# Optimization experiments

Measured on AMD Instinct MI355X. Metric: run time of the kernel, lower is better.

Reference implementation:

```python
import jax, jax.numpy as jnp
import numpy as np
from math import comb

# Implicit Bernstein form (BERN-NN-Implicit): a polynomial in V vars is a stack of
# term blocks; each term = V rows of univariate Bernstein coefficients, poly value
# = sum over terms of the product over vars of the univariate Bernstein polys.
N_IN, T_IN, V, DEG = 16, 64, 4, 4
C = DEG + 1          # coeffs per row at degree DEG
K = 2 * DEG + 1      # coeffs per row at degree 2*DEG (after squaring)

def _prod_matrix(d):
    # Bernstein product: (deg d) x (deg d) -> deg 2d ; c_k = sum_{i+j=k} b_i b_j C(d,i)C(d,j)/C(2d,k)
    M = np.zeros((d + 1, d + 1, 2 * d + 1), np.float32)
    for i in range(d + 1):
        for j in range(d + 1):
            M[i, j, i + j] = comb(d, i) * comb(d, j) / comb(2 * d, i + j)
    return jnp.asarray(M)

def _elev_matrix(d):
    # degree elevation d -> 2d : b'_j = sum_i b_i C(d,i)C(d,j-i)/C(2d,j)
    E = np.zeros((d + 1, 2 * d + 1), np.float32)
    for i in range(d + 1):
        for j in range(i, i + d + 1):
            E[i, j] = comb(d, i) * comb(d, j - i) / comb(2 * d, j)
    return jnp.asarray(E)

M_PROD = _prod_matrix(DEG)
E_ELEV = _elev_matrix(DEG)

def _scaled_terms(polys, w, idx):
    # mult_with_constant fused over all contributing inputs: scale row 0 of each term
    # block by the (nonzero) weight; concat of term blocks == sum_2_polys at equal degree.
    if idx.size == 0:
        return jnp.zeros((1, V, C), polys.dtype)  # zero polynomial (one zero term)
    sel = polys[idx]                                   # (n, T, V, C)
    sel = sel.at[:, :, 0, :].multiply(w[idx][:, None, None])
    return sel.reshape(-1, V, C)

def _add_const(P, c):
    # add_with_constant: append a constant term (Bernstein coeffs of a constant are all c)
    cols = P.shape[-1]
    row0 = c * jnp.ones((1, 1, cols), P.dtype)
    rest = jnp.ones((1, V - 1, cols), P.dtype)
    return jnp.concatenate([P, jnp.concatenate([row0, rest], axis=1)], axis=0)

def _ibf_minmax(P):
    # per-term interval = product over vars of [min,max] of each row; sum over terms
    lo = P.min(axis=-1); hi = P.max(axis=-1)           # (T, V)
    tlo, thi = lo[:, 0], hi[:, 0]
    for v in range(1, V):
        cands = jnp.stack([tlo * lo[:, v], tlo * hi[:, v], thi * lo[:, v], thi * hi[:, v]])
        tlo, thi = cands.min(0), cands.max(0)
    return tlo.sum(), thi.sum()

def _quad_of_poly(P, a, b, c):
    # a*p^2 + b*p + c in implicit Bernstein form; p^2 = all pairwise term products
    T = P.shape[0]
    sq = jnp.einsum('avi,bvj,ijk->abvk', P, P, M_PROD).reshape(T * T, V, K)
    sq = sq.at[:, 0, :].multiply(a)
    lin = jnp.einsum('tvi,ij->tvj', P, E_ELEV)          # elevate DEG -> 2*DEG
    lin = lin.at[:, 0, :].multiply(b)
    const = jnp.concatenate([c * jnp.ones((1, 1, K)), jnp.ones((1, V - 1, K))], axis=1)
    return jnp.concatenate([sq, lin, const], axis=0)

def _node_io(under_in, over_in, pos_w, neg_w, bias, pos_idx, neg_idx):
    under = jnp.concatenate([_scaled_terms(over_in, neg_w, neg_idx),
                             _scaled_terms(under_in, pos_w, pos_idx)], axis=0)
    under = _add_const(under, bias)
    over = jnp.concatenate([_scaled_terms(over_in, pos_w, pos_idx),
                            _scaled_terms(under_in, neg_w, neg_idx)], axis=0)
    over = _add_const(over, bias)
    return under, over

def setup_inputs() -> dict:
    key = jax.random.key(0)
    k1, k2, k3 = jax.random.split(key, 3)
    ui = 0.5 * jax.random.normal(k1, (N_IN, T_IN, V, C), jnp.float32)
    oi = ui + 0.05 * jnp.abs(jax.random.normal(k2, (N_IN, T_IN, V, C), jnp.float32))
    w = jax.random.normal(k3, (N_IN,), jnp.float32)
    return {
        'layer_inputs_under': ui,
        'layer_inputs_over': oi,
        'node_pos_weights': jnp.maximum(w, 0.0),
        'node_neg_weights': jnp.minimum(w, 0.0),
        'node_bias': jnp.asarray(-0.1, jnp.float32),
        'layer_inputs_under_degrees': jnp.full((N_IN, V), DEG, jnp.int32),
        'layer_inputs_over_degrees': jnp.full((N_IN, V), DEG, jnp.int32),
    }

def reference(layer_inputs_under, layer_inputs_over, node_pos_weights, node_neg_weights,
              node_bias, layer_inputs_under_degrees, layer_inputs_over_degrees):
    pos_idx = np.nonzero(np.asarray(node_pos_weights))[0]
    neg_idx = np.nonzero(np.asarray(node_neg_weights))[0]
    under, over = _node_io(layer_inputs_under, layer_inputs_over,
                           node_pos_weights, node_neg_weights, node_bias, pos_idx, neg_idx)
    deg = jnp.maximum(layer_inputs_under_degrees.astype(jnp.float32).max(0),
                      layer_inputs_over_degrees.astype(jnp.float32).max(0))  # (V,)
    l = _ibf_minmax(under)[0]
    u = _ibf_minmax(over)[1]
    lf, uf = float(l), float(u)   # host sync, mirrors the original's data-dependent branch
    if uf <= 0.0:
        return (jnp.zeros((1,)), jnp.zeros((1,)), jnp.zeros(V), jnp.zeros(V))
    if lf >= 0.0:
        return (under.reshape(-1, C), over.reshape(-1, C), deg, deg)
    # mixed case: sound quadratic relaxation of ReLU on [l, u]
    a, b, c = 1.0 / (-4.0 * l), 0.5, -l / 4.0   # upper: (x - l)^2 / (-4 l) >= relu(x)
    over_q = _quad_of_poly(over, a, b, c).reshape(-1, K)
    if uf >= -lf:
        # under relaxation = identity (coeffs [0,1,0])
        return (under.reshape(-1, C), over_q, deg, 2.0 * deg)
    # under relaxation = 0 (coeffs all zero)
    return (jnp.zeros((V, 1)), over_q, jnp.zeros(V), 2.0 * deg)
```

## Files before the change

### kernel.cpp

```cpp
#include <hip/hip_runtime.h>

#define NINP 16
#define TIN 64
#define NV 4
#define NC 5
#define NK 9
#define T_ROWS 1025
#define NPAIR (1025 * 1025)
#define UNDER_SZ (T_ROWS * NV * NC)
#define OQ_OFF UNDER_SZ
#define OQ_SQ_SZ (NPAIR * NV * NK)
#define TAIL_ELEMS ((T_ROWS + 1) * NV * NK)
#define DEG_OFF (OQ_OFF + OQ_SQ_SZ + TAIL_ELEMS)
#define WS_POVER 0
#define L_PART_LL 10252
#define FIXED_SCALE 16777216.0f

#define PREP_ELEM_BLOCKS 161
#define PREP_L_BLOCKS 4
#define PAIR_BLOCKS 4105
#define TAIL_BLOCKS 145

__device__ __forceinline__ int count_nz16(const float* __restrict__ w) {
    int c = 0;
#pragma unroll
    for (int n = 0; n < NINP; n++) c += (w[n] != 0.0f) ? 1 : 0;
    return c;
}

__device__ __forceinline__ int kth_nz16(const float* __restrict__ w, int k) {
    int c = 0, r = 0;
#pragma unroll
    for (int n = 0; n < NINP; n++) {
        bool nz = (w[n] != 0.0f);
        if (nz && c == k) r = n;
        c += nz ? 1 : 0;
    }
    return r;
}

__device__ __forceinline__ float under_val(const float* __restrict__ ui,
                                           const float* __restrict__ oi,
                                           const float* __restrict__ posw,
                                           const float* __restrict__ negw,
                                           float bias, int r, int v, int c) {
    if (r < 1024) {
        int g = r >> 6, tt = r & 63;
        int nNeg = count_nz16(negw);
        if (g < nNeg) {
            int n = kth_nz16(negw, g);
            return oi[((n * TIN + tt) * NV + v) * NC + c] * ((v == 0) ? negw[n] : 1.0f);
        }
        int n = kth_nz16(posw, g - nNeg);
        return ui[((n * TIN + tt) * NV + v) * NC + c] * ((v == 0) ? posw[n] : 1.0f);
    }
    return (v == 0) ? bias : 1.0f;
}

__global__ __launch_bounds__(256) void prep_kernel(
    const float* __restrict__ ui, const float* __restrict__ oi,
    const float* __restrict__ posw, const float* __restrict__ negw,
    const float* __restrict__ bias,
    const int* __restrict__ udeg, const int* __restrict__ odeg,
    float* __restrict__ out, float* __restrict__ ws) {
    const int bid = blockIdx.x;
    const int t = threadIdx.x;

    if (bid < PREP_ELEM_BLOCKS) {
        int gid = bid * 256 + t;
        if (gid < NV) {
            int m = 0;
            for (int n = 0; n < NINP; n++) {
                int a = udeg[n * NV + gid];
                int b = odeg[n * NV + gid];
                m = max(m, max(a, b));
            }
            out[DEG_OFF + gid] = (float)m;
            out[DEG_OFF + NV + gid] = 2.0f * (float)m;
        }
        if (gid < UNDER_SZ) {
            int r = gid / 20, rem = gid - r * 20, v = rem / 5, c = rem - v * 5;
            out[gid] = under_val(ui, oi, posw, negw, bias[0], r, v, c);
        } else if (gid < 2 * UNDER_SZ) {
            int e = gid - UNDER_SZ;
            int r = e / 20, rem = e - r * 20, v = rem / 5, c = rem - v * 5;
            float val;
            if (r < 1024) {
                int g = r >> 6, tt = r & 63;
                int nPos = count_nz16(posw);
                if (g < nPos) {
                    int n = kth_nz16(posw, g);
                    val = oi[((n * TIN + tt) * NV + v) * NC + c] * ((v == 0) ? posw[n] : 1.0f);
                } else {
                    int n = kth_nz16(negw, g - nPos);
                    val = ui[((n * TIN + tt) * NV + v) * NC + c] * ((v == 0) ? negw[n] : 1.0f);
                }
            } else {
                val = (v == 0) ? bias[0] : 1.0f;
            }
            ws[WS_POVER + e] = val;
        }
    } else {
        __shared__ long long s[256];
        const float b0 = bias[0];
        int r = (bid - PREP_ELEM_BLOCKS) * 256 + t;
        float tlo = 0.f, thi = 0.f;
#pragma unroll
        for (int v = 0; v < NV; v++) {
            float lo = under_val(ui, oi, posw, negw, b0, r, v, 0), hi = lo;
#pragma unroll
            for (int c = 1; c < NC; c++) {
                float x = under_val(ui, oi, posw, negw, b0, r, v, c);
                lo = fminf(lo, x);
                hi = fmaxf(hi, x);
            }
            if (v == 0) { tlo = lo; thi = hi; }
            else {
                float p0 = tlo * lo, p1 = tlo * hi, p2 = thi * lo, p3 = thi * hi;
                tlo = fminf(fminf(p0, p1), fminf(p2, p3));
                thi = fmaxf(fmaxf(p0, p1), fmaxf(p2, p3));
            }
        }
        long long acc = __float2ll_rn(tlo * FIXED_SCALE);
        if (bid == PREP_ELEM_BLOCKS && t == 0) {
            acc += __float2ll_rn(b0 * FIXED_SCALE);
        }
        s[t] = acc;
        __syncthreads();
        for (int off = 128; off > 0; off >>= 1) {
            if (t < off) s[t] += s[t + off];
            __syncthreads();
        }
        if (t == 0) ((long long*)ws)[L_PART_LL + (bid - PREP_ELEM_BLOCKS)] = s[0];
    }
}

__device__ __forceinline__ float c4_of(int j) {
    if (j == 0 || j == 4) return 1.f;
    if (j == 1 || j == 3) return 4.f;
    if (j == 2) return 6.f;
    return 0.f;
}

__global__ __launch_bounds__(256) void main_kernel(const float* __restrict__ P,
                                                   const long long* __restrict__ lpart,
                                                   float* __restrict__ out) {
    const int bid = blockIdx.x;
    const int t = threadIdx.x;
    const long long ll = lpart[0] + lpart[1] + lpart[2] + lpart[3];
    const float l = (float)ll * (1.0f / FIXED_SCALE);

    if (bid < PAIR_BLOCKS) {
        __shared__ float lds[256 * 37];
        const int p0 = bid * 256;
        int nvalid = NPAIR - p0;
        if (nvalid > 256) nvalid = 256;
        const float ascale = -0.25f / l;

        if (t < nvalid) {
            int p = p0 + t;
            int ai = p / 1025;
            int bi = p - ai * 1025;
            float pa[20], pb[20];
            const float4* A4 = reinterpret_cast<const float4*>(P + ai * 20);
            const float4* B4 = reinterpret_cast<const float4*>(P + bi * 20);
#pragma unroll
            for (int q = 0; q < 5; q++) {
                float4 x = A4[q];
                pa[4 * q] = x.x; pa[4 * q + 1] = x.y; pa[4 * q + 2] = x.z; pa[4 * q + 3] = x.w;
                float4 y = B4[q];
                pb[4 * q] = y.x; pb[4 * q + 1] = y.y; pb[4 * q + 2] = y.z; pb[4 * q + 3] = y.w;
            }
            const float C4[5] = {1.f, 4.f, 6.f, 4.f, 1.f};
            const float invC8[9] = {1.f, 0.125f, 1.f / 28.f, 1.f / 56.f, 1.f / 70.f,
                                    1.f / 56.f, 1.f / 28.f, 0.125f, 1.f};
#pragma unroll
            for (int v = 0; v < NV; v++) {
                float a_[5], b_[5];
#pragma unroll
                for (int i = 0; i < 5; i++) {
                    a_[i] = pa[v * 5 + i] * C4[i];
                    b_[i] = pb[v * 5 + i] * C4[i];
                }
                float cc[9];
#pragma unroll
                for (int k = 0; k < 9; k++) cc[k] = 0.f;
#pragma unroll
                for (int i = 0; i < 5; i++)
#pragma unroll
                    for (int j = 0; j < 5; j++) cc[i + j] += a_[i] * b_[j];
                const float sc = (v == 0) ? ascale : 1.0f;
#pragma unroll
                for (int k = 0; k < 9; k++) lds[t * 37 + v * 9 + k] = cc[k] * invC8[k] * sc;
            }
        }
        __syncthreads();

        const int nf4 = nvalid * 9;
        float4* out4 = reinterpret_cast<float4*>(out) + (5125 + (long)p0 * 9);
        int f4 = t;
        int pl = t / 9, w4 = (t % 9) * 4;
        for (; f4 < nf4; f4 += 256) {
            float4 r;
            r.x = lds[pl * 37 + w4];
            r.y = lds[pl * 37 + w4 + 1];
            r.z = lds[pl * 37 + w4 + 2];
            r.w = lds[pl * 37 + w4 + 3];
            out4[f4] = r;
            pl += 28; w4 += 16;
            if (w4 >= 36) { w4 -= 36; pl++; }
        }
    } else {
        int idx = (bid - PAIR_BLOCKS) * 256 + t;
        if (idx >= TAIL_ELEMS) return;
        int rl = idx / 36, rem = idx - rl * 36, v = rem / 9, k = rem - v * 9;
        const float invC8[9] = {1.f, 0.125f, 1.f / 28.f, 1.f / 56.f, 1.f / 70.f,
                                1.f / 56.f, 1.f / 28.f, 0.125f, 1.f};
        const float C4[5] = {1.f, 4.f, 6.f, 4.f, 1.f};
        float val;
        if (rl < T_ROWS) {
            float acc = 0.f;
#pragma unroll
            for (int i = 0; i < 5; i++) {
                float e = C4[i] * c4_of(k - i);
                acc += P[rl * 20 + v * 5 + i] * e;
            }
            val = acc * invC8[k] * ((v == 0) ? 0.5f : 1.0f);
        } else {
            val = (v == 0) ? (-0.25f * l) : 1.0f;
        }
        out[OQ_OFF + (long)NPAIR * 36 + idx] = val;
    }
}

extern "C" void kernel_launch(void* const* d_in, const int* in_sizes, int n_in,
                              void* d_out, int out_size, void* d_ws, size_t ws_size,
                              hipStream_t stream) {
    const float* ui   = (const float*)d_in[0];
    const float* oi   = (const float*)d_in[1];
    const float* posw = (const float*)d_in[2];
    const float* negw = (const float*)d_in[3];
    const float* bias = (const float*)d_in[4];
    const int*   udeg = (const int*)d_in[5];
    const int*   odeg = (const int*)d_in[6];
    float* out = (float*)d_out;
    float* ws  = (float*)d_ws;

    prep_kernel<<<PREP_ELEM_BLOCKS + PREP_L_BLOCKS, 256, 0, stream>>>(
        ui, oi, posw, negw, bias, udeg, odeg, out, ws);
    main_kernel<<<PAIR_BLOCKS + TAIL_BLOCKS, 256, 0, stream>>>(
        ws + WS_POVER, ((const long long*)ws) + L_PART_LL, out);
}
```

Baseline: 43.81 us.

## Split each pair's variables across two threads and stream output in two phases

Each pair product is now computed by two threads, each handling two of the four variables, and each block processes its 256 pairs in two phases of 128 with half-size LDS. Output is written as scalar floats with a strided loop rather than float4 stores. The aim is more parallelism per pair, less register pressure and LDS per block, and higher occupancy. The trade-off is an extra barrier per phase and narrower global stores, which may cost write bandwidth.

```diff
diff --git a/kernel.cpp b/kernel.cpp
--- a/kernel.cpp
+++ b/kernel.cpp
@@ -147,68 +147,73 @@
                                                    float* __restrict__ out) {
     const int bid = blockIdx.x;
     const int t = threadIdx.x;
-    const long long ll = lpart[0] + lpart[1] + lpart[2] + lpart[3];
-    const float l = (float)ll * (1.0f / FIXED_SCALE);
+    const long long llv = lpart[0] + lpart[1] + lpart[2] + lpart[3];
+    const float l = (float)llv * (1.0f / FIXED_SCALE);
 
     if (bid < PAIR_BLOCKS) {
-        __shared__ float lds[256 * 37];
-        const int p0 = bid * 256;
-        int nvalid = NPAIR - p0;
-        if (nvalid > 256) nvalid = 256;
+        __shared__ float lds[128 * 37];
         const float ascale = -0.25f / l;
-
-        if (t < nvalid) {
-            int p = p0 + t;
-            int ai = p / 1025;
-            int bi = p - ai * 1025;
-            float pa[20], pb[20];
-            const float4* A4 = reinterpret_cast<const float4*>(P + ai * 20);
-            const float4* B4 = reinterpret_cast<const float4*>(P + bi * 20);
-#pragma unroll
-            for (int q = 0; q < 5; q++) {
-                float4 x = A4[q];
-                pa[4 * q] = x.x; pa[4 * q + 1] = x.y; pa[4 * q + 2] = x.z; pa[4 * q + 3] = x.w;
-                float4 y = B4[q];
-                pb[4 * q] = y.x; pb[4 * q + 1] = y.y; pb[4 * q + 2] = y.z; pb[4 * q + 3] = y.w;
-            }
-            const float C4[5] = {1.f, 4.f, 6.f, 4.f, 1.f};
-            const float invC8[9] = {1.f, 0.125f, 1.f / 28.f, 1.f / 56.f, 1.f / 70.f,
-                                    1.f / 56.f, 1.f / 28.f, 0.125f, 1.f};
-#pragma unroll
-            for (int v = 0; v < NV; v++) {
-                float a_[5], b_[5];
-#pragma unroll
-                for (int i = 0; i < 5; i++) {
-                    a_[i] = pa[v * 5 + i] * C4[i];
-                    b_[i] = pb[v * 5 + i] * C4[i];
-                }
-                float cc[9];
-#pragma unroll
-                for (int k = 0; k < 9; k++) cc[k] = 0.f;
-#pragma unroll
-                for (int i = 0; i < 5; i++)
-#pragma unroll
-                    for (int j = 0; j < 5; j++) cc[i + j] += a_[i] * b_[j];
-                const float sc = (v == 0) ? ascale : 1.0f;
-#pragma unroll
-                for (int k = 0; k < 9; k++) lds[t * 37 + v * 9 + k] = cc[k] * invC8[k] * sc;
-            }
-        }
-        __syncthreads();
-
-        const int nf4 = nvalid * 9;
-        float4* out4 = reinterpret_cast<float4*>(out) + (5125 + (long)p0 * 9);
-        int f4 = t;
-        int pl = t / 9, w4 = (t % 9) * 4;
-        for (; f4 < nf4; f4 += 256) {
-            float4 r;
-            r.x = lds[pl * 37 + w4];
-            r.y = lds[pl * 37 + w4 + 1];
-            r.z = lds[pl * 37 + w4 + 2];
-            r.w = lds[pl * 37 + w4 + 3];
-            out4[f4] = r;
-            pl += 28; w4 += 16;
-            if (w4 >= 36) { w4 -= 36; pl++; }
+        const int pi = t >> 1;
+        const int h = t & 1;
+        const float invC8[9] = {1.f, 0.125f, 1.f / 28.f, 1.f / 56.f, 1.f / 70.f,
+                                1.f / 56.f, 1.f / 28.f, 0.125f, 1.f};
+
+#pragma unroll 2
+        for (int ph = 0; ph < 2; ph++) {
+            const int p0 = bid * 256 + ph * 128;
+            int nv_ = NPAIR - p0;
+            nv_ = (nv_ < 0) ? 0 : ((nv_ > 128) ? 128 : nv_);
+
+            if (pi < nv_) {
+                const int p = p0 + pi;
+                const int ai = p / 1025;
+                const int bi = p - ai * 1025;
+                const float* rA = P + ai * 20 + h * 10;
+                const float* rB = P + bi * 20 + h * 10;
+                float a_[10], b_[10];
+#pragma unroll
+                for (int e = 0; e < 5; e++) {
+                    float2 x = *reinterpret_cast<const float2*>(rA + 2 * e);
+                    a_[2 * e] = x.x; a_[2 * e + 1] = x.y;
+                    float2 y = *reinterpret_cast<const float2*>(rB + 2 * e);
+                    b_[2 * e] = y.x; b_[2 * e + 1] = y.y;
+                }
+#pragma unroll
+                for (int s = 0; s < 2; s++) {
+#pragma unroll
+                    for (int i = 0; i < 5; i++) {
+                        const float c4 = (i == 0 || i == 4) ? 1.f : ((i == 2) ? 6.f : 4.f);
+                        a_[5 * s + i] *= c4;
+                        b_[5 * s + i] *= c4;
+                    }
+                }
+#pragma unroll
+                for (int s = 0; s < 2; s++) {
+                    const float sc = (h == 0 && s == 0) ? ascale : 1.0f;
+                    float cc[9];
+#pragma unroll
+                    for (int k = 0; k < 9; k++) cc[k] = 0.f;
+#pragma unroll
+                    for (int i = 0; i < 5; i++)
+#pragma unroll
+                        for (int j = 0; j < 5; j++) cc[i + j] += a_[5 * s + i] * b_[5 * s + j];
+#pragma unroll
+                    for (int k = 0; k < 9; k++)
+                        lds[pi * 37 + 18 * h + 9 * s + k] = cc[k] * invC8[k] * sc;
+                }
+            }
+            __syncthreads();
+
+            const int nflt = nv_ * 36;
+            const long base = (long)OQ_OFF + (long)p0 * 36;
+            int f = t;
+            int pl = f / 36, w = f - pl * 36;
+            for (; f < nflt; f += 256) {
+                out[base + f] = lds[pl * 37 + w];
+                pl += 7; w += 4;
+                if (w >= 36) { w -= 36; pl++; }
+            }
+            if (ph == 0) __syncthreads();
         }
     } else {
         int idx = (bid - PAIR_BLOCKS) * 256 + t;
```

New measurement: 44.62 us. About the same (+1.9%).

## Pre-scale binomials in prep and store pair products directly without LDS staging

Applied to the files above, without the earlier changes.

The prep kernel now multiplies the over-polynomial coefficients by the C(4,i) binomial weights, which removes those multiplies from the pair kernel. The tail kernel is adjusted to match. The pair kernel drops the shared-memory transpose and barrier. Each thread now writes its 36 outputs as nine float4 stores, which gives strided per-thread writes instead of fully coalesced block writes. The change trades LDS traffic and synchronisation for less coalesced global stores, on a kernel that is dominated by writing about 150MB of output.

```diff
diff --git a/kernel.cpp b/kernel.cpp
--- a/kernel.cpp
+++ b/kernel.cpp
@@ -98,7 +98,8 @@
             } else {
                 val = (v == 0) ? bias[0] : 1.0f;
             }
-            ws[WS_POVER + e] = val;
+            const float c4 = (c == 0 || c == 4) ? 1.f : ((c == 2) ? 6.f : 4.f);
+            ws[WS_POVER + e] = val * c4;
         }
     } else {
         __shared__ long long s[256];
@@ -147,83 +148,59 @@
                                                    float* __restrict__ out) {
     const int bid = blockIdx.x;
     const int t = threadIdx.x;
-    const long long ll = lpart[0] + lpart[1] + lpart[2] + lpart[3];
-    const float l = (float)ll * (1.0f / FIXED_SCALE);
+    const long long llv = lpart[0] + lpart[1] + lpart[2] + lpart[3];
+    const float l = (float)llv * (1.0f / FIXED_SCALE);
 
     if (bid < PAIR_BLOCKS) {
-        __shared__ float lds[256 * 37];
-        const int p0 = bid * 256;
-        int nvalid = NPAIR - p0;
-        if (nvalid > 256) nvalid = 256;
+        const int p = bid * 256 + t;
+        if (p >= NPAIR) return;
         const float ascale = -0.25f / l;
-
-        if (t < nvalid) {
-            int p = p0 + t;
-            int ai = p / 1025;
-            int bi = p - ai * 1025;
-            float pa[20], pb[20];
-            const float4* A4 = reinterpret_cast<const float4*>(P + ai * 20);
-            const float4* B4 = reinterpret_cast<const float4*>(P + bi * 20);
-#pragma unroll
-            for (int q = 0; q < 5; q++) {
-                float4 x = A4[q];
-                pa[4 * q] = x.x; pa[4 * q + 1] = x.y; pa[4 * q + 2] = x.z; pa[4 * q + 3] = x.w;
-                float4 y = B4[q];
-                pb[4 * q] = y.x; pb[4 * q + 1] = y.y; pb[4 * q + 2] = y.z; pb[4 * q + 3] = y.w;
-            }
-            const float C4[5] = {1.f, 4.f, 6.f, 4.f, 1.f};
-            const float invC8[9] = {1.f, 0.125f, 1.f / 28.f, 1.f / 56.f, 1.f / 70.f,
-                                    1.f / 56.f, 1.f / 28.f, 0.125f, 1.f};
-#pragma unroll
-            for (int v = 0; v < NV; v++) {
-                float a_[5], b_[5];
-#pragma unroll
-                for (int i = 0; i < 5; i++) {
-                    a_[i] = pa[v * 5 + i] * C4[i];
-                    b_[i] = pb[v * 5 + i] * C4[i];
-                }
-                float cc[9];
-#pragma unroll
-                for (int k = 0; k < 9; k++) cc[k] = 0.f;
-#pragma unroll
-                for (int i = 0; i < 5; i++)
-#pragma unroll
-                    for (int j = 0; j < 5; j++) cc[i + j] += a_[i] * b_[j];
-                const float sc = (v == 0) ? ascale : 1.0f;
-#pragma unroll
-                for (int k = 0; k < 9; k++) lds[t * 37 + v * 9 + k] = cc[k] * invC8[k] * sc;
-            }
-        }
-        __syncthreads();
-
-        const int nf4 = nvalid * 9;
-        float4* out4 = reinterpret_cast<float4*>(out) + (5125 + (long)p0 * 9);
-        int f4 = t;
-        int pl = t / 9, w4 = (t % 9) * 4;
-        for (; f4 < nf4; f4 += 256) {
-            float4 r;
-            r.x = lds[pl * 37 + w4];
-            r.y = lds[pl * 37 + w4 + 1];
-            r.z = lds[pl * 37 + w4 + 2];
-            r.w = lds[pl * 37 + w4 + 3];
-            out4[f4] = r;
-            pl += 28; w4 += 16;
-            if (w4 >= 36) { w4 -= 36; pl++; }
-        }
+        const int ai = p / 1025;
+        const int bi = p - ai * 1025;
+        float pa[20], pb[20];
+        const float4* A4 = reinterpret_cast<const float4*>(P + ai * 20);
+        const float4* B4 = reinterpret_cast<const float4*>(P + bi * 20);
+#pragma unroll
+        for (int q = 0; q < 5; q++) {
+            float4 x = A4[q];
+            pa[4 * q] = x.x; pa[4 * q + 1] = x.y; pa[4 * q + 2] = x.z; pa[4 * q + 3] = x.w;
+            float4 y = B4[q];
+            pb[4 * q] = y.x; pb[4 * q + 1] = y.y; pb[4 * q + 2] = y.z; pb[4 * q + 3] = y.w;
+        }
+#pragma unroll
+        for (int i = 0; i < 5; i++) pa[i] *= ascale;
+
+        const float invC8[9] = {1.f, 0.125f, 1.f / 28.f, 1.f / 56.f, 1.f / 70.f,
+                                1.f / 56.f, 1.f / 28.f, 0.125f, 1.f};
+        float o[36];
+#pragma unroll
+        for (int v = 0; v < NV; v++) {
+            float cc[9];
+#pragma unroll
+            for (int k = 0; k < 9; k++) cc[k] = 0.f;
+#pragma unroll
+            for (int i = 0; i < 5; i++)
+#pragma unroll
+                for (int j = 0; j < 5; j++) cc[i + j] += pa[v * 5 + i] * pb[v * 5 + j];
+#pragma unroll
+            for (int k = 0; k < 9; k++) o[v * 9 + k] = cc[k] * invC8[k];
+        }
+        float4* out4 = reinterpret_cast<float4*>(out) + (5125 + p * 9);
+#pragma unroll
+        for (int q = 0; q < 9; q++)
+            out4[q] = make_float4(o[4 * q], o[4 * q + 1], o[4 * q + 2], o[4 * q + 3]);
     } else {
         int idx = (bid - PAIR_BLOCKS) * 256 + t;
         if (idx >= TAIL_ELEMS) return;
         int rl = idx / 36, rem = idx - rl * 36, v = rem / 9, k = rem - v * 9;
         const float invC8[9] = {1.f, 0.125f, 1.f / 28.f, 1.f / 56.f, 1.f / 70.f,
                                 1.f / 56.f, 1.f / 28.f, 0.125f, 1.f};
-        const float C4[5] = {1.f, 4.f, 6.f, 4.f, 1.f};
         float val;
         if (rl < T_ROWS) {
             float acc = 0.f;
 #pragma unroll
             for (int i = 0; i < 5; i++) {
-                float e = C4[i] * c4_of(k - i);
-                acc += P[rl * 20 + v * 5 + i] * e;
+                acc += P[rl * 20 + v * 5 + i] * c4_of(k - i);
             }
             val = acc * invC8[k] * ((v == 0) ? 0.5f : 1.0f);
         } else {
```

New measurement: 71.68 us. 1.64x slower.
